# Kernel optimization log

Hardware: AMD Instinct MI355X
Metric: run time of the kernel (lower is better)

The kernel has to match this reference:

```python
import jax, jax.numpy as jnp
import numpy as np

TAU = 0.1
EPS = 1e-8


def setup_inputs() -> dict:
    key = jax.random.key(0)
    k1, k2, k3 = jax.random.split(key, 3)
    B, D = 4096, 256
    features = jax.random.normal(k1, (B, D), dtype=jnp.float32)
    pos_features = jax.random.normal(k2, (B, D), dtype=jnp.float32)
    labels = jax.random.randint(k3, (B,), 0, 64, dtype=jnp.int64)
    return {"features": features, "pos_features": pos_features, "labels": labels}


def reference(features, pos_features, labels):
    # concat image and positive features / duplicate labels
    f = jnp.concatenate([features, pos_features], axis=0)          # [N, D], N = 2B
    lab = jnp.concatenate([labels, labels], axis=0)                # [N]
    N = f.shape[0]

    # cosine similarity: mm(a, a.T) / clamp(w * w.T, 1e-8)
    w = jnp.linalg.norm(f, axis=1, keepdims=True)                  # [N, 1]
    logits = (f @ f.T) / jnp.clip(w * w.T, EPS)                    # [N, N]
    z = logits / TAU

    diag = jnp.eye(N, dtype=bool)
    neg_inf = jnp.asarray(-jnp.inf, dtype=z.dtype)

    # denominator: logsumexp over all off-diagonal entries per row
    loss_all = jnp.sum(jax.nn.logsumexp(jnp.where(diag, neg_inf, z), axis=1))

    # positives: for each row, logsumexp over same-label off-diagonal entries.
    # This vectorizes the original python loop over unique labels: the union of
    # the per-label sub-matrices (diagonal removed) is exactly this mask.
    same = (lab[:, None] == lab[None, :]) & ~diag                  # [N, N]
    loss_pos = jnp.sum(jax.nn.logsumexp(jnp.where(same, z, neg_inf), axis=1))

    return loss_all - loss_pos
```

## Files before the change

### kernel.cpp

```cpp
#include <hip/hip_runtime.h>
#include <hip/hip_bf16.h>
#include <stdint.h>

#define NROWS 8192
#define DDIM  256
#define BM    128
#define BN    128
#define BK    32
#define NTILE (NROWS / BM)
#define NTRI  (NTILE * (NTILE + 1) / 2)
#define L2E   1.44269504088896340736f

#define COL_STRIDE2 5
#define ROW_STRIDE2 18
#define ROWAP_OFF   5120
#define SMEM_BYTES  (ROWAP_OFF + 128 * ROW_STRIDE2 * 8)

typedef __attribute__((ext_vector_type(8))) short short8;
typedef __attribute__((ext_vector_type(4))) float f32x4;

typedef const __attribute__((address_space(1))) uint32_t glb_u32;
typedef __attribute__((address_space(3))) uint32_t lds_u32;

__device__ __forceinline__ void load_lds16(const unsigned short* g, unsigned short* l) {
  __builtin_amdgcn_global_load_lds((glb_u32*)g, (lds_u32*)l, 16, 0, 0);
}

__device__ __forceinline__ unsigned short f2bf(float x) {
  __hip_bfloat16 h = __float2bfloat16(x);
  return *reinterpret_cast<unsigned short*>(&h);
}

__global__ void __launch_bounds__(256)
milnce_prep(const float* __restrict__ feat, const float* __restrict__ pos,
            const int* __restrict__ labels, unsigned short* __restrict__ fb,
            float* __restrict__ inv_w, int* __restrict__ lab,
            float* __restrict__ S_all, float* __restrict__ S_pos) {
  const int wave = threadIdx.x >> 6;
  const int lane = threadIdx.x & 63;
  const int row  = blockIdx.x * 4 + wave;

  const float* src = (row < 4096) ? (feat + (size_t)row * DDIM)
                                  : (pos + (size_t)(row - 4096) * DDIM);
  float4 v = ((const float4*)src)[lane];

  ushort4 o;
  o.x = f2bf(v.x); o.y = f2bf(v.y); o.z = f2bf(v.z); o.w = f2bf(v.w);
  ((ushort4*)(fb + (size_t)row * DDIM))[lane] = o;

  float ss = v.x*v.x + v.y*v.y + v.z*v.z + v.w*v.w;
  #pragma unroll
  for (int m = 1; m < 64; m <<= 1) ss += __shfl_xor(ss, m, 64);
  if (lane == 0) inv_w[row] = 1.0f / sqrtf(ss);

  const int tid = blockIdx.x * 256 + threadIdx.x;
  if (tid < NROWS) {
    lab[tid]   = labels[tid & 4095];
    S_all[tid] = 0.0f;
    S_pos[tid] = 0.0f;
  }
}

__global__ void __launch_bounds__(256)
milnce_gemm(const unsigned short* __restrict__ fb, const float* __restrict__ inv_w,
            const int* __restrict__ lab, float* __restrict__ S_all,
            float* __restrict__ S_pos) {
  __shared__ __align__(16) char smem[SMEM_BYTES];
  unsigned short* ldsA = (unsigned short*)smem;
  unsigned short* ldsB = (unsigned short*)(smem + 8192);
  float2* colAP = (float2*)smem;
  float2* rowAP = (float2*)(smem + ROWAP_OFF);

  int t = blockIdx.x, d = 0, rem = NTILE;
  while (t >= rem) { t -= rem; ++d; --rem; }
  const int bi = t, bj = t + d;

  const int tid  = threadIdx.x;
  const int wave = tid >> 6;
  const int lane = tid & 63;
  const int quad = lane >> 4;
  const int l15  = lane & 15;
  const int wm   = wave >> 1;
  const int wn   = wave & 1;
  const int rowBase = bi * BM;
  const int colBase = bj * BN;

  f32x4 acc[4][4];
  #pragma unroll
  for (int i = 0; i < 4; ++i)
    #pragma unroll
    for (int j = 0; j < 4; ++j) acc[i][j] = (f32x4){0.f, 0.f, 0.f, 0.f};

  const int s0 = wave * 64 + lane;
  const int s1 = s0 + 256;
  const int r0 = s0 >> 2, g0 = (s0 & 3) ^ ((s0 >> 3) & 3);
  const int r1 = s1 >> 2, g1 = (s1 & 3) ^ ((s1 >> 3) & 3);
  const unsigned short* gA0 = fb + (size_t)(rowBase + r0) * DDIM + g0 * 8;
  const unsigned short* gA1 = fb + (size_t)(rowBase + r1) * DDIM + g1 * 8;
  const unsigned short* gB0 = fb + (size_t)(colBase + r0) * DDIM + g0 * 8;
  const unsigned short* gB1 = fb + (size_t)(colBase + r1) * DDIM + g1 * 8;
  unsigned short* lA0 = ldsA + (size_t)(wave * 64) * 8;
  unsigned short* lA1 = ldsA + (size_t)(wave * 64 + 256) * 8;
  unsigned short* lB0 = ldsB + (size_t)(wave * 64) * 8;
  unsigned short* lB1 = ldsB + (size_t)(wave * 64 + 256) * 8;

  const int xsl = quad ^ ((l15 >> 1) & 3);

  #pragma unroll
  for (int kt = 0; kt < DDIM / BK; ++kt) {
    const int ko = kt * BK;
    __syncthreads();
    load_lds16(gA0 + ko, lA0);
    load_lds16(gA1 + ko, lA1);
    load_lds16(gB0 + ko, lB0);
    load_lds16(gB1 + ko, lB1);
    __syncthreads();

    short8 a[4], b[4];
    #pragma unroll
    for (int mi = 0; mi < 4; ++mi)
      a[mi] = *(const short8*)&ldsA[(wm * 64 + mi * 16 + l15) * BK + xsl * 8];
    #pragma unroll
    for (int ni = 0; ni < 4; ++ni)
      b[ni] = *(const short8*)&ldsB[(wn * 64 + ni * 16 + l15) * BK + xsl * 8];

    #pragma unroll
    for (int mi = 0; mi < 4; ++mi)
      #pragma unroll
      for (int ni = 0; ni < 4; ++ni)
        acc[mi][ni] = __builtin_amdgcn_mfma_f32_16x16x32_bf16(a[mi], b[ni], acc[mi][ni], 0, 0, 0);
  }

  __syncthreads();

  const float SHIFT = 10.0f * L2E;
  float cf[4]; int cl[4], colg[4];
  #pragma unroll
  for (int ni = 0; ni < 4; ++ni) {
    colg[ni] = colBase + wn * 64 + ni * 16 + l15;
    cf[ni]   = inv_w[colg[ni]] * (10.0f * L2E);
    cl[ni]   = lab[colg[ni]];
  }

  const bool offdiag = (bi != bj);

  float2 capk[4] = {{0.f,0.f},{0.f,0.f},{0.f,0.f},{0.f,0.f}};

  if (offdiag) {
    #pragma unroll
    for (int mi = 0; mi < 4; ++mi) {
      const int rbase = wm * 64 + mi * 16 + quad * 4;
      const float4 rf4 = *(const float4*)&inv_w[rowBase + rbase];
      const int4   rl4 = *(const int4*)&lab[rowBase + rbase];
      #pragma unroll
      for (int r = 0; r < 4; ++r) {
        const float rf = (r == 0) ? rf4.x : (r == 1) ? rf4.y : (r == 2) ? rf4.z : rf4.w;
        const int   rl = (r == 0) ? rl4.x : (r == 1) ? rl4.y : (r == 2) ? rl4.z : rl4.w;
        float sx = 0.f, sy = 0.f;
        #pragma unroll
        for (int ni = 0; ni < 4; ++ni) {
          float e  = exp2f(acc[mi][ni][r] * rf * cf[ni] - SHIFT);
          float ep = (rl == cl[ni]) ? e : 0.f;
          capk[ni].x += e; capk[ni].y += ep;
          sx += e; sy += ep;
        }
        rowAP[(rbase + r) * ROW_STRIDE2 + wn * 16 + l15] = make_float2(sx, sy);
      }
    }
  } else {
    #pragma unroll
    for (int mi = 0; mi < 4; ++mi) {
      const int rbase = wm * 64 + mi * 16 + quad * 4;
      const float4 rf4 = *(const float4*)&inv_w[rowBase + rbase];
      const int4   rl4 = *(const int4*)&lab[rowBase + rbase];
      #pragma unroll
      for (int r = 0; r < 4; ++r) {
        const float rf = (r == 0) ? rf4.x : (r == 1) ? rf4.y : (r == 2) ? rf4.z : rf4.w;
        const int   rl = (r == 0) ? rl4.x : (r == 1) ? rl4.y : (r == 2) ? rl4.z : rl4.w;
        const int rowg = rowBase + rbase + r;
        #pragma unroll
        for (int ni = 0; ni < 4; ++ni) {
          float e = exp2f(acc[mi][ni][r] * rf * cf[ni] - SHIFT);
          if (rowg == colg[ni]) e = 0.f;
          float ep = (rl == cl[ni]) ? e : 0.f;
          capk[ni].x += e; capk[ni].y += ep;
        }
      }
    }
  }

  #pragma unroll
  for (int ni = 0; ni < 4; ++ni)
    colAP[(wn * 64 + ni * 16 + l15) * COL_STRIDE2 + quad] = capk[ni];

  __syncthreads();

  if (tid < 128) {
    const float2* cp = &colAP[tid * COL_STRIDE2];
    float2 c0 = cp[0], c1 = cp[1], c2 = cp[2], c3 = cp[3];
    float sx = (c0.x + c1.x) + (c2.x + c3.x);
    float sy = (c0.y + c1.y) + (c2.y + c3.y);
    atomicAdd(&S_all[colBase + tid], sx);
    atomicAdd(&S_pos[colBase + tid], sy);
  } else if (offdiag) {
    const int rr = tid - 128;
    const float2* rp = &rowAP[rr * ROW_STRIDE2];
    float sx = 0.f, sy = 0.f;
    #pragma unroll
    for (int i = 0; i < 16; ++i) { sx += rp[i].x; sy += rp[i].y; }
    atomicAdd(&S_all[rowBase + rr], sx);
    atomicAdd(&S_pos[rowBase + rr], sy);
  }
}

__global__ void __launch_bounds__(1024)
milnce_final(const float* __restrict__ S_all, const float* __restrict__ S_pos,
             float* __restrict__ out) {
  __shared__ float red[16];
  float s = 0.f;
  for (int i = threadIdx.x; i < NROWS; i += 1024)
    s += logf(S_all[i]) - logf(S_pos[i]);
  #pragma unroll
  for (int m = 1; m < 64; m <<= 1) s += __shfl_xor(s, m, 64);
  const int wave = threadIdx.x >> 6;
  if ((threadIdx.x & 63) == 0) red[wave] = s;
  __syncthreads();
  if (threadIdx.x == 0) {
    float t = 0.f;
    #pragma unroll
    for (int i = 0; i < 16; ++i) t += red[i];
    out[0] = t;
  }
}

extern "C" void kernel_launch(void* const* d_in, const int* in_sizes, int n_in,
                              void* d_out, int out_size, void* d_ws, size_t ws_size,
                              hipStream_t stream) {
  const float* feat   = (const float*)d_in[0];
  const float* pos    = (const float*)d_in[1];
  const int*   labels = (const int*)d_in[2];

  char* ws = (char*)d_ws;
  unsigned short* fb    = (unsigned short*)ws;
  float*          inv_w = (float*)(ws + 4u * 1024 * 1024);
  int*            lab   = (int*)  (ws + 4u * 1024 * 1024 + 32 * 1024);
  float*          S_all = (float*)(ws + 4u * 1024 * 1024 + 64 * 1024);
  float*          S_pos = (float*)(ws + 4u * 1024 * 1024 + 96 * 1024);
  float*          out   = (float*)d_out;

  hipLaunchKernelGGL(milnce_prep, dim3(NROWS / 4), dim3(256), 0, stream,
                     feat, pos, labels, fb, inv_w, lab, S_all, S_pos);
  hipLaunchKernelGGL(milnce_gemm, dim3(NTRI), dim3(256), 0, stream,
                     fb, inv_w, lab, S_all, S_pos);
  hipLaunchKernelGGL(milnce_final, dim3(1), dim3(1024), 0, stream,
                     S_all, S_pos, out);
}
```

Measured before the change: 106.1 us.

## Fuse final reduction into GEMM via last-block counter, widen BK to 64

Raises the GEMM K-tile from 32 to 64 with a new 8-way XOR swizzle, halving the number of barrier-separated load/compute steps. Drops the separate final reduction kernel: the last GEMM block, found through an atomic done counter, computes the log-sum. Labels are now read directly from the input rather than copied into a workspace array. The changes save a launch and some sync overhead, but double LDS use per block, which may lower occupancy.

New measurement: 139.3 us. 31.3% more time.

```diff
diff --git a/kernel.cpp b/kernel.cpp
--- a/kernel.cpp
+++ b/kernel.cpp
@@ -6,7 +6,7 @@
 #define DDIM  256
 #define BM    128
 #define BN    128
-#define BK    32
+#define BK    64
 #define NTILE (NROWS / BM)
 #define NTRI  (NTILE * (NTILE + 1) / 2)
 #define L2E   1.44269504088896340736f
@@ -14,7 +14,12 @@
 #define COL_STRIDE2 5
 #define ROW_STRIDE2 18
 #define ROWAP_OFF   5120
-#define SMEM_BYTES  (ROWAP_OFF + 128 * ROW_STRIDE2 * 8)
+#define SMEM_BYTES  32768
+
+#define WS_INVW (4u * 1024 * 1024)
+#define WS_SALL (WS_INVW + 32 * 1024)
+#define WS_SPOS (WS_SALL + 32 * 1024)
+#define WS_DONE (WS_SPOS + 32 * 1024)
 
 typedef __attribute__((ext_vector_type(8))) short short8;
 typedef __attribute__((ext_vector_type(4))) float f32x4;
@@ -33,9 +38,9 @@
 
 __global__ void __launch_bounds__(256)
 milnce_prep(const float* __restrict__ feat, const float* __restrict__ pos,
-            const int* __restrict__ labels, unsigned short* __restrict__ fb,
-            float* __restrict__ inv_w, int* __restrict__ lab,
-            float* __restrict__ S_all, float* __restrict__ S_pos) {
+            unsigned short* __restrict__ fb, float* __restrict__ inv_w,
+            float* __restrict__ S_all, float* __restrict__ S_pos,
+            unsigned int* __restrict__ done) {
   const int wave = threadIdx.x >> 6;
   const int lane = threadIdx.x & 63;
   const int row  = blockIdx.x * 4 + wave;
@@ -54,22 +59,22 @@
   if (lane == 0) inv_w[row] = 1.0f / sqrtf(ss);
 
   const int tid = blockIdx.x * 256 + threadIdx.x;
-  if (tid < NROWS) {
-    lab[tid]   = labels[tid & 4095];
-    S_all[tid] = 0.0f;
-    S_pos[tid] = 0.0f;
-  }
+  if (tid < NROWS) { S_all[tid] = 0.0f; S_pos[tid] = 0.0f; }
+  if (tid == 0) *done = 0u;
 }
 
 __global__ void __launch_bounds__(256)
 milnce_gemm(const unsigned short* __restrict__ fb, const float* __restrict__ inv_w,
-            const int* __restrict__ lab, float* __restrict__ S_all,
-            float* __restrict__ S_pos) {
+            const int* __restrict__ labels, float* __restrict__ S_all,
+            float* __restrict__ S_pos, unsigned int* __restrict__ done,
+            float* __restrict__ out) {
   __shared__ __align__(16) char smem[SMEM_BYTES];
   unsigned short* ldsA = (unsigned short*)smem;
-  unsigned short* ldsB = (unsigned short*)(smem + 8192);
+  unsigned short* ldsB = (unsigned short*)(smem + 16384);
   float2* colAP = (float2*)smem;
   float2* rowAP = (float2*)(smem + ROWAP_OFF);
+  unsigned int* lastFlag = (unsigned int*)(smem + 24064);
+  float* red = (float*)(smem + 24128);
 
   int t = blockIdx.x, d = 0, rem = NTILE;
   while (t >= rem) { t -= rem; ++d; --rem; }
@@ -91,44 +96,40 @@
     #pragma unroll
     for (int j = 0; j < 4; ++j) acc[i][j] = (f32x4){0.f, 0.f, 0.f, 0.f};
 
-  const int s0 = wave * 64 + lane;
-  const int s1 = s0 + 256;
-  const int r0 = s0 >> 2, g0 = (s0 & 3) ^ ((s0 >> 3) & 3);
-  const int r1 = s1 >> 2, g1 = (s1 & 3) ^ ((s1 >> 3) & 3);
-  const unsigned short* gA0 = fb + (size_t)(rowBase + r0) * DDIM + g0 * 8;
-  const unsigned short* gA1 = fb + (size_t)(rowBase + r1) * DDIM + g1 * 8;
-  const unsigned short* gB0 = fb + (size_t)(colBase + r0) * DDIM + g0 * 8;
-  const unsigned short* gB1 = fb + (size_t)(colBase + r1) * DDIM + g1 * 8;
-  unsigned short* lA0 = ldsA + (size_t)(wave * 64) * 8;
-  unsigned short* lA1 = ldsA + (size_t)(wave * 64 + 256) * 8;
-  unsigned short* lB0 = ldsB + (size_t)(wave * 64) * 8;
-  unsigned short* lB1 = ldsB + (size_t)(wave * 64 + 256) * 8;
-
-  const int xsl = quad ^ ((l15 >> 1) & 3);
+  const int srow = tid >> 3;
+  const int gsl  = (tid & 7) ^ (srow & 7);
+  const unsigned short* baseA = fb + (size_t)(rowBase + srow) * DDIM + gsl * 8;
+  const unsigned short* baseB = fb + (size_t)(colBase + srow) * DDIM + gsl * 8;
+  unsigned short* lbA = ldsA + wave * 512;
+  unsigned short* lbB = ldsB + wave * 512;
 
   #pragma unroll
   for (int kt = 0; kt < DDIM / BK; ++kt) {
-    const int ko = kt * BK;
     __syncthreads();
-    load_lds16(gA0 + ko, lA0);
-    load_lds16(gA1 + ko, lA1);
-    load_lds16(gB0 + ko, lB0);
-    load_lds16(gB1 + ko, lB1);
+    #pragma unroll
+    for (int r = 0; r < 4; ++r) {
+      load_lds16(baseA + r * (32 * DDIM) + kt * BK, lbA + r * 2048);
+      load_lds16(baseB + r * (32 * DDIM) + kt * BK, lbB + r * 2048);
+    }
     __syncthreads();
 
-    short8 a[4], b[4];
-    #pragma unroll
-    for (int mi = 0; mi < 4; ++mi)
-      a[mi] = *(const short8*)&ldsA[(wm * 64 + mi * 16 + l15) * BK + xsl * 8];
-    #pragma unroll
-    for (int ni = 0; ni < 4; ++ni)
-      b[ni] = *(const short8*)&ldsB[(wn * 64 + ni * 16 + l15) * BK + xsl * 8];
-
-    #pragma unroll
-    for (int mi = 0; mi < 4; ++mi)
+    #pragma unroll
+    for (int h = 0; h < 2; ++h) {
+      const int xsl = ((h * 4 + quad) ^ (l15 & 7)) * 8;
+      short8 a[4], b[4];
+      #pragma unroll
+      for (int mi = 0; mi < 4; ++mi)
+        a[mi] = *(const short8*)&ldsA[(wm * 64 + mi * 16 + l15) * BK + xsl];
       #pragma unroll
       for (int ni = 0; ni < 4; ++ni)
-        acc[mi][ni] = __builtin_amdgcn_mfma_f32_16x16x32_bf16(a[mi], b[ni], acc[mi][ni], 0, 0, 0);
+        b[ni] = *(const short8*)&ldsB[(wn * 64 + ni * 16 + l15) * BK + xsl];
+
+      #pragma unroll
+      for (int mi = 0; mi < 4; ++mi)
+        #pragma unroll
+        for (int ni = 0; ni < 4; ++ni)
+          acc[mi][ni] = __builtin_amdgcn_mfma_f32_16x16x32_bf16(a[mi], b[ni], acc[mi][ni], 0, 0, 0);
+    }
   }
 
   __syncthreads();
@@ -139,7 +140,7 @@
   for (int ni = 0; ni < 4; ++ni) {
     colg[ni] = colBase + wn * 64 + ni * 16 + l15;
     cf[ni]   = inv_w[colg[ni]] * (10.0f * L2E);
-    cl[ni]   = lab[colg[ni]];
+    cl[ni]   = labels[colg[ni] & 4095];
   }
 
   const bool offdiag = (bi != bj);
@@ -151,7 +152,7 @@
     for (int mi = 0; mi < 4; ++mi) {
       const int rbase = wm * 64 + mi * 16 + quad * 4;
       const float4 rf4 = *(const float4*)&inv_w[rowBase + rbase];
-      const int4   rl4 = *(const int4*)&lab[rowBase + rbase];
+      const int4   rl4 = *(const int4*)&labels[(rowBase + rbase) & 4095];
       #pragma unroll
       for (int r = 0; r < 4; ++r) {
         const float rf = (r == 0) ? rf4.x : (r == 1) ? rf4.y : (r == 2) ? rf4.z : rf4.w;
@@ -172,7 +173,7 @@
     for (int mi = 0; mi < 4; ++mi) {
       const int rbase = wm * 64 + mi * 16 + quad * 4;
       const float4 rf4 = *(const float4*)&inv_w[rowBase + rbase];
-      const int4   rl4 = *(const int4*)&lab[rowBase + rbase];
+      const int4   rl4 = *(const int4*)&labels[(rowBase + rbase) & 4095];
       #pragma unroll
       for (int r = 0; r < 4; ++r) {
         const float rf = (r == 0) ? rf4.x : (r == 1) ? rf4.y : (r == 2) ? rf4.z : rf4.w;
@@ -211,25 +212,26 @@
     atomicAdd(&S_all[rowBase + rr], sx);
     atomicAdd(&S_pos[rowBase + rr], sy);
   }
-}
-
-__global__ void __launch_bounds__(1024)
-milnce_final(const float* __restrict__ S_all, const float* __restrict__ S_pos,
-             float* __restrict__ out) {
-  __shared__ float red[16];
-  float s = 0.f;
-  for (int i = threadIdx.x; i < NROWS; i += 1024)
-    s += logf(S_all[i]) - logf(S_pos[i]);
-  #pragma unroll
-  for (int m = 1; m < 64; m <<= 1) s += __shfl_xor(s, m, 64);
-  const int wave = threadIdx.x >> 6;
-  if ((threadIdx.x & 63) == 0) red[wave] = s;
-  __syncthreads();
-  if (threadIdx.x == 0) {
-    float t = 0.f;
-    #pragma unroll
-    for (int i = 0; i < 16; ++i) t += red[i];
-    out[0] = t;
+
+  __syncthreads();
+  if (tid == 0) {
+    __threadfence();
+    *lastFlag = (atomicAdd(done, 1u) == NTRI - 1) ? 1u : 0u;
+  }
+  __syncthreads();
+  if (*lastFlag) {
+    __threadfence();
+    float s = 0.f;
+    for (int i = tid; i < NROWS; i += 256) {
+      float sa = __hip_atomic_load(&S_all[i], __ATOMIC_RELAXED, __HIP_MEMORY_SCOPE_AGENT);
+      float sp = __hip_atomic_load(&S_pos[i], __ATOMIC_RELAXED, __HIP_MEMORY_SCOPE_AGENT);
+      s += __logf(sa) - __logf(sp);
+    }
+    #pragma unroll
+    for (int m = 1; m < 64; m <<= 1) s += __shfl_xor(s, m, 64);
+    if (lane == 0) red[wave] = s;
+    __syncthreads();
+    if (tid == 0) out[0] = (red[0] + red[1]) + (red[2] + red[3]);
   }
 }
 
@@ -242,16 +244,14 @@
 
   char* ws = (char*)d_ws;
   unsigned short* fb    = (unsigned short*)ws;
-  float*          inv_w = (float*)(ws + 4u * 1024 * 1024);
-  int*            lab   = (int*)  (ws + 4u * 1024 * 1024 + 32 * 1024);
-  float*          S_all = (float*)(ws + 4u * 1024 * 1024 + 64 * 1024);
-  float*          S_pos = (float*)(ws + 4u * 1024 * 1024 + 96 * 1024);
+  float*          inv_w = (float*)(ws + WS_INVW);
+  float*          S_all = (float*)(ws + WS_SALL);
+  float*          S_pos = (float*)(ws + WS_SPOS);
+  unsigned int*   done  = (unsigned int*)(ws + WS_DONE);
   float*          out   = (float*)d_out;
 
   hipLaunchKernelGGL(milnce_prep, dim3(NROWS / 4), dim3(256), 0, stream,
-                     feat, pos, labels, fb, inv_w, lab, S_all, S_pos);
+                     feat, pos, fb, inv_w, S_all, S_pos, done);
   hipLaunchKernelGGL(milnce_gemm, dim3(NTRI), dim3(256), 0, stream,
-                     fb, inv_w, lab, S_all, S_pos);
-  hipLaunchKernelGGL(milnce_final, dim3(1), dim3(1024), 0, stream,
-                     S_all, S_pos, out);
-}
+                     fb, inv_w, labels, S_all, S_pos, done, out);
+}
```
